# Performance work log

Measured on AMD Instinct MI355X. Metric: run time of the kernel, lower is better.

## Reference

```python
import jax, jax.numpy as jnp
import numpy as np

N_NODES = 100000
N_EDGES = 1600000
IN_DIM, HID_DIM, OUT_DIM = 128, 64, 32


def gcn_conv(x, edge_index, W, b, n_nodes):
    """PyG GCNConv: add self-loops, symmetric deg^-1/2 normalization,
    linear transform, gather->scatter-sum aggregation, then bias."""
    loops = jnp.arange(n_nodes, dtype=edge_index.dtype)
    src = jnp.concatenate([edge_index[0], loops])  # [E+N]
    dst = jnp.concatenate([edge_index[1], loops])  # [E+N]
    # degree over targets (includes self-loops)
    deg = jax.ops.segment_sum(jnp.ones_like(dst, dtype=x.dtype), dst,
                              num_segments=n_nodes)
    dinv = jnp.where(deg > 0, jax.lax.rsqrt(deg), 0.0)
    norm = dinv[src] * dinv[dst]                   # [E+N]
    h = x @ W                                      # [N, F_out]
    msg = h[src] * norm[:, None]                   # gather + scale
    out = jax.ops.segment_sum(msg, dst, num_segments=n_nodes)
    return out + b


def setup_inputs() -> dict:
    key = jax.random.key(0)
    k1, k2, k3, k4 = jax.random.split(key, 4)
    x = jax.random.normal(k1, (N_NODES, IN_DIM), dtype=jnp.float32)
    edge_index = jax.random.randint(k2, (2, N_EDGES), 0, N_NODES,
                                    dtype=jnp.int64)
    # Glorot-ish init for weights, zero bias (PyG default: glorot + zeros)
    W1 = jax.random.normal(k3, (IN_DIM, HID_DIM), dtype=jnp.float32) * (1.0 / np.sqrt(IN_DIM))
    b1 = jnp.zeros((HID_DIM,), dtype=jnp.float32)
    W2 = jax.random.normal(k4, (HID_DIM, OUT_DIM), dtype=jnp.float32) * (1.0 / np.sqrt(HID_DIM))
    b2 = jnp.zeros((OUT_DIM,), dtype=jnp.float32)
    return {"x": x, "edge_index": edge_index, "W1": W1, "b1": b1,
            "W2": W2, "b2": b2}


def reference(x, edge_index, W1, b1, W2, b2):
    n = x.shape[0]
    h = jax.nn.relu(gcn_conv(x, edge_index, W1, b1, n))
    return gcn_conv(h, edge_index, W2, b2, n)
```

## Files before the change

kernel.cpp:

```cpp
#include <hip/hip_runtime.h>


#define BLK 256
#define BLKC 1024
#define EPT 8
#define CITER 18
#define BSHIFT 10
#define NPB 1024
#define SLOTB 18432
#define NBMAX 128

typedef unsigned int uint_t;
typedef unsigned short ushort_t;
typedef __attribute__((ext_vector_type(2))) float v2f;
typedef __attribute__((ext_vector_type(8))) short bf16x8;
typedef __attribute__((ext_vector_type(4))) float f32x4;

__device__ __forceinline__ uint_t pkbf(float lo, float hi) {
    uint_t r;
    asm("v_cvt_pk_bf16_f32 %0, %1, %2" : "=v"(r) : "v"(lo), "v"(hi));
    return r;
}

__device__ __forceinline__ void pkadd(v2f& a0, v2f& a1, v2f& a2, v2f& a3, uint4 v) {
    v2f p;
    p.x = __uint_as_float(v.x << 16); p.y = __uint_as_float(v.x & 0xffff0000u); a0 += p;
    p.x = __uint_as_float(v.y << 16); p.y = __uint_as_float(v.y & 0xffff0000u); a1 += p;
    p.x = __uint_as_float(v.z << 16); p.y = __uint_as_float(v.z & 0xffff0000u); a2 += p;
    p.x = __uint_as_float(v.w << 16); p.y = __uint_as_float(v.w & 0xffff0000u); a3 += p;
}

__device__ __forceinline__ bool detect64(const int* __restrict__ idx) {
    int z = 0;
#pragma unroll
    for (int i = 1; i < 32; i += 2) z |= idx[i];
    return z == 0;
}

__global__ void k_part(const int* __restrict__ idx, int* __restrict__ bcursor,
                       int* __restrict__ edge_part,
                       const float* __restrict__ W1, const float* __restrict__ W2,
                       ushort_t* __restrict__ wt, int E, int nbuck, int PB) {
    if (blockIdx.x == PB) {
        int t = threadIdx.x;
        int n = t >> 2, q = t & 3;
        uint_t buf[16];
#pragma unroll
        for (int i = 0; i < 16; ++i) {
            float a = W1[(size_t)(32 * q + 2 * i) * 64 + n];
            float b = W1[(size_t)(32 * q + 2 * i + 1) * 64 + n];
            buf[i] = pkbf(a, b);
        }
#pragma unroll
        for (int i = 0; i < 4; ++i)
            ((uint4*)wt)[(size_t)n * 16 + q * 4 + i] = *(uint4*)&buf[4 * i];
        if (t < 128) {
            int n2 = t >> 2, q2 = t & 3;
            uint_t b2[8];
#pragma unroll
            for (int i = 0; i < 8; ++i) {
                float a = W2[(size_t)(16 * q2 + 2 * i) * 32 + n2];
                float b = W2[(size_t)(16 * q2 + 2 * i + 1) * 32 + n2];
                b2[i] = pkbf(a, b);
            }
#pragma unroll
            for (int i = 0; i < 2; ++i)
                ((uint4*)(wt + 8192))[(size_t)n2 * 8 + q2 * 2 + i] = *(uint4*)&b2[4 * i];
        }
        return;
    }
    __shared__ int h[NBMAX];
    __shared__ int rb[NBMAX];
    bool is64 = detect64(idx);
    int t = threadIdx.x, blk = blockIdx.x;
    for (int i = t; i < nbuck; i += BLK) h[i] = 0;
    __syncthreads();
    int base = blk * (BLK * EPT) + t;
    int dst[EPT], src[EPT], rk[EPT];
#pragma unroll
    for (int k = 0; k < EPT; ++k) {
        int e = base + k * BLK;
        if (e < E) {
            if (is64) {
                uint2 dv = ((const uint2*)idx)[(size_t)E + e];
                uint2 sv = ((const uint2*)idx)[e];
                dst[k] = (int)dv.x;
                src[k] = (int)sv.x;
            } else {
                dst[k] = idx[E + e];
                src[k] = idx[e];
            }
            rk[k] = atomicAdd(&h[dst[k] >> BSHIFT], 1);
        } else {
            dst[k] = -1;
        }
    }
    __syncthreads();
    for (int i = t; i < nbuck; i += BLK) {
        int c = h[i];
        rb[i] = c ? atomicAdd(&bcursor[i], c) : 0;
    }
    __syncthreads();
#pragma unroll
    for (int k = 0; k < EPT; ++k) {
        if (dst[k] >= 0) {
            int b = dst[k] >> BSHIFT;
            edge_part[(size_t)b * SLOTB + rb[b] + rk[k]] =
                src[k] | ((dst[k] & (NPB - 1)) << 17);
        }
    }
}

__global__ __launch_bounds__(BLKC) void k_csr(
        const int* __restrict__ edge_part, const int* __restrict__ bcursor,
        int* __restrict__ row_ptr, int* __restrict__ deg, float* __restrict__ dinv,
        int* __restrict__ csr_src, int N, int nbuck) {
    __shared__ int cnt[NPB];
    __shared__ int off[NPB];
    __shared__ int wsum[16];
    int b = blockIdx.x, t = threadIdx.x;
    int node0 = b << BSHIFT;
    int nn = min(NPB, N - node0);
    int m = bcursor[b];
    size_t ebase = (size_t)b * SLOTB;
    cnt[t] = 0;
    __syncthreads();
    int pp[CITER], rr[CITER];
#pragma unroll
    for (int it = 0; it < CITER; ++it) {
        int e = t + it * BLKC;
        if (e < m) {
            int p = edge_part[ebase + e];
            pp[it] = p;
            rr[it] = atomicAdd(&cnt[((unsigned)p) >> 17], 1);
        }
    }
    __syncthreads();
    int cown = cnt[t];
    int xi = cown;
#pragma unroll
    for (int d = 1; d < 64; d <<= 1) {
        int y = __shfl_up(xi, d, 64);
        if ((t & 63) >= d) xi += y;
    }
    if ((t & 63) == 63) wsum[t >> 6] = xi;
    __syncthreads();
    if (t < 16) {
        int wv = wsum[t];
#pragma unroll
        for (int d = 1; d < 16; d <<= 1) {
            int y = __shfl_up(wv, d, 64);
            if (t >= d) wv += y;
        }
        wsum[t] = wv;
    }
    __syncthreads();
    int excl = xi - cown + ((t >= 64) ? wsum[(t >> 6) - 1] : 0);
    off[t] = excl;
    if (t < nn) {
        row_ptr[node0 + t] = (int)(ebase + excl);
        deg[node0 + t] = cown;
        dinv[node0 + t] = rsqrtf((float)(cown + 1));
    }
    __syncthreads();
#pragma unroll
    for (int it = 0; it < CITER; ++it) {
        int e = t + it * BLKC;
        if (e < m) {
            int p = pp[it];
            int dlo = ((unsigned)p) >> 17;
            csr_src[ebase + off[dlo] + rr[it]] = p & 0x1FFFF;
        }
    }
}

__global__ __launch_bounds__(256) void k_gemm1(
        const float* __restrict__ x, const ushort_t* __restrict__ wt,
        const float* __restrict__ dinv, ushort_t* __restrict__ hs1, int N) {
    __shared__ ushort_t xb[64][136];
    __shared__ ushort_t wb[64][136];
    int t = threadIdx.x;
    int rbase = blockIdx.x * 64;
    for (int i = t; i < 1024; i += BLK) {
        int n = i >> 4, q = i & 15;
        uint4 v = ((const uint4*)wt)[i];
        *(uint4*)&wb[n][8 * q] = v;
    }
    for (int i = t; i < 2048; i += BLK) {
        int r = i >> 5, c4 = i & 31;
        int rr = rbase + r; if (rr >= N) rr = N - 1;
        float4 v = ((const float4*)x)[(size_t)rr * 32 + c4];
        uint2 p;
        p.x = pkbf(v.x, v.y);
        p.y = pkbf(v.z, v.w);
        *(uint2*)&xb[r][4 * c4] = p;
    }
    __syncthreads();
    int w = t >> 6, l = t & 63;
    int lane16 = l & 15, quad = l >> 4;
    int mrow = 16 * w + lane16;
    f32x4 acc0 = {0.f, 0.f, 0.f, 0.f}, acc1 = {0.f, 0.f, 0.f, 0.f};
    f32x4 acc2 = {0.f, 0.f, 0.f, 0.f}, acc3 = {0.f, 0.f, 0.f, 0.f};
#pragma unroll
    for (int kk = 0; kk < 4; ++kk) {
        int k0 = kk * 32 + quad * 8;
        bf16x8 a  = *(const bf16x8*)&xb[mrow][k0];
        bf16x8 b0 = *(const bf16x8*)&wb[lane16][k0];
        bf16x8 b1 = *(const bf16x8*)&wb[lane16 + 16][k0];
        bf16x8 b2 = *(const bf16x8*)&wb[lane16 + 32][k0];
        bf16x8 b3 = *(const bf16x8*)&wb[lane16 + 48][k0];
        acc0 = __builtin_amdgcn_mfma_f32_16x16x32_bf16(a, b0, acc0, 0, 0, 0);
        acc1 = __builtin_amdgcn_mfma_f32_16x16x32_bf16(a, b1, acc1, 0, 0, 0);
        acc2 = __builtin_amdgcn_mfma_f32_16x16x32_bf16(a, b2, acc2, 0, 0, 0);
        acc3 = __builtin_amdgcn_mfma_f32_16x16x32_bf16(a, b3, acc3, 0, 0, 0);
    }
    __syncthreads();
    int orow = 16 * w + quad * 4;
    float d0 = dinv[min(rbase + orow + 0, N - 1)];
    float d1 = dinv[min(rbase + orow + 1, N - 1)];
    float d2 = dinv[min(rbase + orow + 2, N - 1)];
    float d3 = dinv[min(rbase + orow + 3, N - 1)];
    uint_t u;
    u = pkbf(acc0.x * d0, acc0.y * d1);
    xb[orow + 0][lane16] = (ushort_t)u;  xb[orow + 1][lane16] = (ushort_t)(u >> 16);
    u = pkbf(acc0.z * d2, acc0.w * d3);
    xb[orow + 2][lane16] = (ushort_t)u;  xb[orow + 3][lane16] = (ushort_t)(u >> 16);
    u = pkbf(acc1.x * d0, acc1.y * d1);
    xb[orow + 0][lane16 + 16] = (ushort_t)u;  xb[orow + 1][lane16 + 16] = (ushort_t)(u >> 16);
    u = pkbf(acc1.z * d2, acc1.w * d3);
    xb[orow + 2][lane16 + 16] = (ushort_t)u;  xb[orow + 3][lane16 + 16] = (ushort_t)(u >> 16);
    u = pkbf(acc2.x * d0, acc2.y * d1);
    xb[orow + 0][lane16 + 32] = (ushort_t)u;  xb[orow + 1][lane16 + 32] = (ushort_t)(u >> 16);
    u = pkbf(acc2.z * d2, acc2.w * d3);
    xb[orow + 2][lane16 + 32] = (ushort_t)u;  xb[orow + 3][lane16 + 32] = (ushort_t)(u >> 16);
    u = pkbf(acc3.x * d0, acc3.y * d1);
    xb[orow + 0][lane16 + 48] = (ushort_t)u;  xb[orow + 1][lane16 + 48] = (ushort_t)(u >> 16);
    u = pkbf(acc3.z * d2, acc3.w * d3);
    xb[orow + 2][lane16 + 48] = (ushort_t)u;  xb[orow + 3][lane16 + 48] = (ushort_t)(u >> 16);
    __syncthreads();
    for (int i = t; i < 512; i += BLK) {
        int r = i >> 3, c8 = i & 7;
        int rr = rbase + r;
        if (rr < N) {
            uint4 v = *(const uint4*)&xb[r][8 * c8];
            *(uint4*)&hs1[(size_t)rr * 64 + 8 * c8] = v;
        }
    }
}

__global__ void k_agg1(const uint_t* __restrict__ hs1, const int* __restrict__ row_ptr,
                       const int* __restrict__ deg, const int* __restrict__ csr_src,
                       const float* __restrict__ dinv, const float* __restrict__ b1,
                       ushort_t* __restrict__ a1b, int N) {
    int lane = threadIdx.x & 63;
    int g = lane >> 3;
    int c = lane & 7;
    int wavebase = ((blockIdx.x * blockDim.x + threadIdx.x) >> 6) * 8;
    int node = wavebase + g;
    bool alive = node < N;
    int nodeC = alive ? node : N - 1;
    const uint4* H = (const uint4*)hs1;
    float dn = dinv[nodeC];
    int beg = row_ptr[nodeC];
    int tot = alive ? deg[nodeC] : 0;
    uint4 selfv = H[(size_t)nodeC * 8 + c];
    int gbase = lane & 0x38;
    int wtot = tot;
    wtot = max(wtot, __shfl_xor(wtot, 8, 64));
    wtot = max(wtot, __shfl_xor(wtot, 16, 64));
    wtot = max(wtot, __shfl_xor(wtot, 32, 64));
    int nch = (wtot + 7) >> 3;
    v2f a0 = {0.f, 0.f}, a1_ = {0.f, 0.f}, a2 = {0.f, 0.f}, a3 = {0.f, 0.f};
    uint4 vA[8], vB[8];
    auto ISSUE = [&](uint4 (&vv)[8], int i) {
        int base = 8 * i;
        int jal = (base + c < tot) ? csr_src[beg + base + c] : 0;
#pragma unroll
        for (int e = 0; e < 8; ++e) {
            int j = __shfl(jal, gbase + e, 64);
            if (base + e < tot) vv[e] = H[(size_t)j * 8 + c];
        }
    };
    auto CONSUME = [&](uint4 (&vv)[8], int i) {
        int base = 8 * i;
#pragma unroll
        for (int e = 0; e < 8; ++e)
            if (base + e < tot) pkadd(a0, a1_, a2, a3, vv[e]);
    };
    if (nch > 0) {
        ISSUE(vA, 0);
        int i = 1;
        for (; i + 1 < nch; i += 2) {
            ISSUE(vB, i);     CONSUME(vA, i - 1);
            ISSUE(vA, i + 1); CONSUME(vB, i);
        }
        if (i < nch) { ISSUE(vB, i); CONSUME(vA, i - 1); CONSUME(vB, i); }
        else          CONSUME(vA, i - 1);
    }
    pkadd(a0, a1_, a2, a3, selfv);
    if (alive) {
        const float4* B = (const float4*)b1;
        float4 bv0 = B[2 * c], bv1 = B[2 * c + 1];
        float o0 = fmaxf(fmaf(a0.x, dn, bv0.x), 0.f);
        float o1 = fmaxf(fmaf(a0.y, dn, bv0.y), 0.f);
        float o2 = fmaxf(fmaf(a1_.x, dn, bv0.z), 0.f);
        float o3 = fmaxf(fmaf(a1_.y, dn, bv0.w), 0.f);
        float o4 = fmaxf(fmaf(a2.x, dn, bv1.x), 0.f);
        float o5 = fmaxf(fmaf(a2.y, dn, bv1.y), 0.f);
        float o6 = fmaxf(fmaf(a3.x, dn, bv1.z), 0.f);
        float o7 = fmaxf(fmaf(a3.y, dn, bv1.w), 0.f);
        uint4 o;
        o.x = pkbf(o0, o1);
        o.y = pkbf(o2, o3);
        o.z = pkbf(o4, o5);
        o.w = pkbf(o6, o7);
        ((uint4*)a1b)[(size_t)node * 8 + c] = o;
    }
}

__global__ __launch_bounds__(256) void k_gemm2(
        const ushort_t* __restrict__ a1b, const ushort_t* __restrict__ wt,
        const float* __restrict__ dinv, ushort_t* __restrict__ hs2, int N) {
    __shared__ ushort_t ab[64][72];
    __shared__ ushort_t wb[32][72];
    int t = threadIdx.x;
    int rbase = blockIdx.x * 64;
    for (int i = t; i < 256; i += BLK) {
        int n = i >> 3, q = i & 7;
        uint4 v = ((const uint4*)(wt + 8192))[i];
        *(uint4*)&wb[n][8 * q] = v;
    }
    for (int i = t; i < 512; i += BLK) {
        int r = i >> 3, c8 = i & 7;
        int rr = rbase + r; if (rr >= N) rr = N - 1;
        uint4 v = ((const uint4*)a1b)[(size_t)rr * 8 + c8];
        *(uint4*)&ab[r][8 * c8] = v;
    }
    __syncthreads();
    int w = t >> 6, l = t & 63;
    int lane16 = l & 15, quad = l >> 4;
    int mrow = 16 * w + lane16;
    f32x4 acc0 = {0.f, 0.f, 0.f, 0.f}, acc1 = {0.f, 0.f, 0.f, 0.f};
#pragma unroll
    for (int kk = 0; kk < 2; ++kk) {
        int k0 = kk * 32 + quad * 8;
        bf16x8 a  = *(const bf16x8*)&ab[mrow][k0];
        bf16x8 b0 = *(const bf16x8*)&wb[lane16][k0];
        bf16x8 b1 = *(const bf16x8*)&wb[lane16 + 16][k0];
        acc0 = __builtin_amdgcn_mfma_f32_16x16x32_bf16(a, b0, acc0, 0, 0, 0);
        acc1 = __builtin_amdgcn_mfma_f32_16x16x32_bf16(a, b1, acc1, 0, 0, 0);
    }
    __syncthreads();
    int orow = 16 * w + quad * 4;
    float d0 = dinv[min(rbase + orow + 0, N - 1)];
    float d1 = dinv[min(rbase + orow + 1, N - 1)];
    float d2 = dinv[min(rbase + orow + 2, N - 1)];
    float d3 = dinv[min(rbase + orow + 3, N - 1)];
    uint_t u;
    u = pkbf(acc0.x * d0, acc0.y * d1);
    ab[orow + 0][lane16] = (ushort_t)u;  ab[orow + 1][lane16] = (ushort_t)(u >> 16);
    u = pkbf(acc0.z * d2, acc0.w * d3);
    ab[orow + 2][lane16] = (ushort_t)u;  ab[orow + 3][lane16] = (ushort_t)(u >> 16);
    u = pkbf(acc1.x * d0, acc1.y * d1);
    ab[orow + 0][lane16 + 16] = (ushort_t)u;  ab[orow + 1][lane16 + 16] = (ushort_t)(u >> 16);
    u = pkbf(acc1.z * d2, acc1.w * d3);
    ab[orow + 2][lane16 + 16] = (ushort_t)u;  ab[orow + 3][lane16 + 16] = (ushort_t)(u >> 16);
    __syncthreads();
    for (int i = t; i < 256; i += BLK) {
        int r = i >> 2, c4 = i & 3;
        int rr = rbase + r;
        if (rr < N) {
            uint4 v = *(const uint4*)&ab[r][8 * c4];
            *(uint4*)&hs2[(size_t)rr * 32 + 8 * c4] = v;
        }
    }
}

__global__ void k_agg2(const uint_t* __restrict__ hs2, const int* __restrict__ row_ptr,
                       const int* __restrict__ deg, const int* __restrict__ csr_src,
                       const float* __restrict__ dinv, const float* __restrict__ b2,
                       float* __restrict__ out, int N) {
    int lane = threadIdx.x & 63;
    int g = lane >> 2;
    int c = lane & 3;
    int wavebase = ((blockIdx.x * blockDim.x + threadIdx.x) >> 6) * 16;
    int node = wavebase + g;
    bool alive = node < N;
    int nodeC = alive ? node : N - 1;
    const uint4* H = (const uint4*)hs2;
    float dn = dinv[nodeC];
    int beg = row_ptr[nodeC];
    int tot = alive ? deg[nodeC] : 0;
    uint4 selfv = H[(size_t)nodeC * 4 + c];
    int gbase = lane & 0x3C;
    int wtot = tot;
    wtot = max(wtot, __shfl_xor(wtot, 4, 64));
    wtot = max(wtot, __shfl_xor(wtot, 8, 64));
    wtot = max(wtot, __shfl_xor(wtot, 16, 64));
    wtot = max(wtot, __shfl_xor(wtot, 32, 64));
    int nch = (wtot + 3) >> 2;
    v2f a0 = {0.f, 0.f}, a1_ = {0.f, 0.f}, a2 = {0.f, 0.f}, a3 = {0.f, 0.f};
    uint4 vA[4], vB[4];
    auto ISSUE = [&](uint4 (&vv)[4], int i) {
        int base = 4 * i;
        int jal = (base + c < tot) ? csr_src[beg + base + c] : 0;
#pragma unroll
        for (int e = 0; e < 4; ++e) {
            int j = __shfl(jal, gbase + e, 64);
            if (base + e < tot) vv[e] = H[(size_t)j * 4 + c];
        }
    };
    auto CONSUME = [&](uint4 (&vv)[4], int i) {
        int base = 4 * i;
#pragma unroll
        for (int e = 0; e < 4; ++e)
            if (base + e < tot) pkadd(a0, a1_, a2, a3, vv[e]);
    };
    if (nch > 0) {
        ISSUE(vA, 0);
        int i = 1;
        for (; i + 1 < nch; i += 2) {
            ISSUE(vB, i);     CONSUME(vA, i - 1);
            ISSUE(vA, i + 1); CONSUME(vB, i);
        }
        if (i < nch) { ISSUE(vB, i); CONSUME(vA, i - 1); CONSUME(vB, i); }
        else          CONSUME(vA, i - 1);
    }
    pkadd(a0, a1_, a2, a3, selfv);
    if (alive) {
        const float4* B = (const float4*)b2;
        float4 bv0 = B[2 * c], bv1 = B[2 * c + 1];
        float4 o0, o1;
        o0.x = fmaf(a0.x, dn, bv0.x);
        o0.y = fmaf(a0.y, dn, bv0.y);
        o0.z = fmaf(a1_.x, dn, bv0.z);
        o0.w = fmaf(a1_.y, dn, bv0.w);
        o1.x = fmaf(a2.x, dn, bv1.x);
        o1.y = fmaf(a2.y, dn, bv1.y);
        o1.z = fmaf(a3.x, dn, bv1.z);
        o1.w = fmaf(a3.y, dn, bv1.w);
        float4* O = (float4*)out;
        O[(size_t)node * 8 + 2 * c] = o0;
        O[(size_t)node * 8 + 2 * c + 1] = o1;
    }
}

extern "C" void kernel_launch(void* const* d_in, const int* in_sizes, int n_in,
                              void* d_out, int out_size, void* d_ws, size_t ws_size,
                              hipStream_t stream) {
    const float* x  = (const float*)d_in[0];
    const int*   idx = (const int*)d_in[1];
    const float* W1 = (const float*)d_in[2];
    const float* b1 = (const float*)d_in[3];
    const float* W2 = (const float*)d_in[4];
    const float* b2 = (const float*)d_in[5];
    float* out = (float*)d_out;

    const int N = in_sizes[0] / 128;
    const int E = in_sizes[1] / 2;
    const int nbuck = (N + NPB - 1) >> BSHIFT;
    const int PB = (E + BLK * EPT - 1) / (BLK * EPT);

    char* ws = (char*)d_ws;
    size_t off = 0;
    auto alloc = [&](size_t bytes) -> char* {
        char* p = ws + off;
        off = (off + bytes + 255) & ~(size_t)255;
        return p;
    };
    float* dinv     = (float*)alloc((size_t)N * 4);
    int*   row_ptr  = (int*)alloc((size_t)N * 4);
    int*   deg      = (int*)alloc((size_t)N * 4);
    int*   bcursor  = (int*)alloc((size_t)nbuck * 4);
    ushort_t* wt    = (ushort_t*)alloc((size_t)(8192 + 2048) * 2);
    int*   csr_src  = (int*)alloc((size_t)nbuck * SLOTB * 4);
    size_t ep_bytes = (size_t)nbuck * SLOTB * 4;
    size_t h1_bytes = (size_t)N * 64 * 2;
    int*   edge_part = (int*)alloc(ep_bytes > h1_bytes ? ep_bytes : h1_bytes);
    ushort_t* a1b   = (ushort_t*)alloc((size_t)N * 64 * 2);
    ushort_t* hs1   = (ushort_t*)edge_part;
    ushort_t* hs2   = hs1;

    hipMemsetAsync(bcursor, 0, (size_t)nbuck * 4, stream);
    k_part<<<PB + 1, BLK, 0, stream>>>(idx, bcursor, edge_part, W1, W2, wt,
                                       E, nbuck, PB);
    k_csr<<<nbuck, BLKC, 0, stream>>>(edge_part, bcursor, row_ptr, deg, dinv,
                                      csr_src, N, nbuck);
    k_gemm1<<<(N + 63) / 64, BLK, 0, stream>>>(x, wt, dinv, hs1, N);
    k_agg1<<<(N * 8 + BLK - 1) / BLK, BLK, 0, stream>>>(
        (const uint_t*)hs1, row_ptr, deg, csr_src, dinv, b1, a1b, N);
    k_gemm2<<<(N + 63) / 64, BLK, 0, stream>>>(a1b, wt, dinv, hs2, N);
    k_agg2<<<(N * 4 + BLK - 1) / BLK, BLK, 0, stream>>>(
        (const uint_t*)hs2, row_ptr, deg, csr_src, dinv, b2, out, N);
}
```

Before: 214.3 us.

## Shrink CSR buckets and use a zero sentinel row for branchless aggregation

Halves the node bucket size (512 nodes per bucket, smaller slot capacity). This gives more k_csr blocks, fewer per-thread iterations and a smaller edge scratch area, with only half the 1024 threads active in the scan phase. The aggregation kernels drop the double-buffered issue/consume pipeline and the per-edge bounds checks. Padding lanes now gather a zero row appended at index N of the hs buffers, which the GEMM kernels write. This removes divergent predication but loses the explicit software prefetch overlap between chunks.

```diff
diff --git a/kernel.cpp b/kernel.cpp
--- a/kernel.cpp
+++ b/kernel.cpp
@@ -4,11 +4,11 @@
 #define BLK 256
 #define BLKC 1024
 #define EPT 8
-#define CITER 18
-#define BSHIFT 10
-#define NPB 1024
-#define SLOTB 18432
-#define NBMAX 128
+#define CITER 10
+#define BSHIFT 9
+#define NPB 512
+#define SLOTB 10240
+#define NBMAX 256
 
 typedef unsigned int uint_t;
 typedef unsigned short ushort_t;
@@ -117,13 +117,13 @@
         int* __restrict__ csr_src, int N, int nbuck) {
     __shared__ int cnt[NPB];
     __shared__ int off[NPB];
-    __shared__ int wsum[16];
+    __shared__ int wsum[8];
     int b = blockIdx.x, t = threadIdx.x;
     int node0 = b << BSHIFT;
     int nn = min(NPB, N - node0);
     int m = bcursor[b];
     size_t ebase = (size_t)b * SLOTB;
-    cnt[t] = 0;
+    if (t < NPB) cnt[t] = 0;
     __syncthreads();
     int pp[CITER], rr[CITER];
 #pragma unroll
@@ -136,31 +136,36 @@
         }
     }
     __syncthreads();
-    int cown = cnt[t];
-    int xi = cown;
-#pragma unroll
-    for (int d = 1; d < 64; d <<= 1) {
-        int y = __shfl_up(xi, d, 64);
-        if ((t & 63) >= d) xi += y;
-    }
-    if ((t & 63) == 63) wsum[t >> 6] = xi;
-    __syncthreads();
-    if (t < 16) {
+    int cown = 0, xi = 0;
+    if (t < NPB) {
+        cown = cnt[t];
+        xi = cown;
+#pragma unroll
+        for (int d = 1; d < 64; d <<= 1) {
+            int y = __shfl_up(xi, d, 64);
+            if ((t & 63) >= d) xi += y;
+        }
+        if ((t & 63) == 63) wsum[t >> 6] = xi;
+    }
+    __syncthreads();
+    if (t < 8) {
         int wv = wsum[t];
 #pragma unroll
-        for (int d = 1; d < 16; d <<= 1) {
+        for (int d = 1; d < 8; d <<= 1) {
             int y = __shfl_up(wv, d, 64);
             if (t >= d) wv += y;
         }
         wsum[t] = wv;
     }
     __syncthreads();
-    int excl = xi - cown + ((t >= 64) ? wsum[(t >> 6) - 1] : 0);
-    off[t] = excl;
-    if (t < nn) {
-        row_ptr[node0 + t] = (int)(ebase + excl);
-        deg[node0 + t] = cown;
-        dinv[node0 + t] = rsqrtf((float)(cown + 1));
+    if (t < NPB) {
+        int excl = xi - cown + ((t >= 64) ? wsum[(t >> 6) - 1] : 0);
+        off[t] = excl;
+        if (t < nn) {
+            row_ptr[node0 + t] = (int)(ebase + excl);
+            deg[node0 + t] = cown;
+            dinv[node0 + t] = rsqrtf((float)(cown + 1));
+        }
     }
     __syncthreads();
 #pragma unroll
@@ -181,6 +186,10 @@
     __shared__ ushort_t wb[64][136];
     int t = threadIdx.x;
     int rbase = blockIdx.x * 64;
+    if (blockIdx.x == 0 && t < 8) {
+        uint4 z = {0u, 0u, 0u, 0u};
+        ((uint4*)hs1)[(size_t)N * 8 + t] = z;
+    }
     for (int i = t; i < 1024; i += BLK) {
         int n = i >> 4, q = i & 15;
         uint4 v = ((const uint4*)wt)[i];
@@ -271,31 +280,18 @@
     wtot = max(wtot, __shfl_xor(wtot, 32, 64));
     int nch = (wtot + 7) >> 3;
     v2f a0 = {0.f, 0.f}, a1_ = {0.f, 0.f}, a2 = {0.f, 0.f}, a3 = {0.f, 0.f};
-    uint4 vA[8], vB[8];
-    auto ISSUE = [&](uint4 (&vv)[8], int i) {
+    for (int i = 0; i < nch; ++i) {
         int base = 8 * i;
-        int jal = (base + c < tot) ? csr_src[beg + base + c] : 0;
+        int jal = (base + c < tot) ? csr_src[beg + base + c] : N;
+        uint4 vv[8];
 #pragma unroll
         for (int e = 0; e < 8; ++e) {
             int j = __shfl(jal, gbase + e, 64);
-            if (base + e < tot) vv[e] = H[(size_t)j * 8 + c];
-        }
-    };
-    auto CONSUME = [&](uint4 (&vv)[8], int i) {
-        int base = 8 * i;
+            vv[e] = H[(size_t)j * 8 + c];
+        }
 #pragma unroll
         for (int e = 0; e < 8; ++e)
-            if (base + e < tot) pkadd(a0, a1_, a2, a3, vv[e]);
-    };
-    if (nch > 0) {
-        ISSUE(vA, 0);
-        int i = 1;
-        for (; i + 1 < nch; i += 2) {
-            ISSUE(vB, i);     CONSUME(vA, i - 1);
-            ISSUE(vA, i + 1); CONSUME(vB, i);
-        }
-        if (i < nch) { ISSUE(vB, i); CONSUME(vA, i - 1); CONSUME(vB, i); }
-        else          CONSUME(vA, i - 1);
+            pkadd(a0, a1_, a2, a3, vv[e]);
     }
     pkadd(a0, a1_, a2, a3, selfv);
     if (alive) {
@@ -325,6 +321,10 @@
     __shared__ ushort_t wb[32][72];
     int t = threadIdx.x;
     int rbase = blockIdx.x * 64;
+    if (blockIdx.x == 0 && t < 4) {
+        uint4 z = {0u, 0u, 0u, 0u};
+        ((uint4*)hs2)[(size_t)N * 4 + t] = z;
+    }
     for (int i = t; i < 256; i += BLK) {
         int n = i >> 3, q = i & 7;
         uint4 v = ((const uint4*)(wt + 8192))[i];
@@ -400,31 +400,18 @@
     wtot = max(wtot, __shfl_xor(wtot, 32, 64));
     int nch = (wtot + 3) >> 2;
     v2f a0 = {0.f, 0.f}, a1_ = {0.f, 0.f}, a2 = {0.f, 0.f}, a3 = {0.f, 0.f};
-    uint4 vA[4], vB[4];
-    auto ISSUE = [&](uint4 (&vv)[4], int i) {
+    for (int i = 0; i < nch; ++i) {
         int base = 4 * i;
-        int jal = (base + c < tot) ? csr_src[beg + base + c] : 0;
+        int jal = (base + c < tot) ? csr_src[beg + base + c] : N;
+        uint4 vv[4];
 #pragma unroll
         for (int e = 0; e < 4; ++e) {
             int j = __shfl(jal, gbase + e, 64);
-            if (base + e < tot) vv[e] = H[(size_t)j * 4 + c];
-        }
-    };
-    auto CONSUME = [&](uint4 (&vv)[4], int i) {
-        int base = 4 * i;
+            vv[e] = H[(size_t)j * 4 + c];
+        }
 #pragma unroll
         for (int e = 0; e < 4; ++e)
-            if (base + e < tot) pkadd(a0, a1_, a2, a3, vv[e]);
-    };
-    if (nch > 0) {
-        ISSUE(vA, 0);
-        int i = 1;
-        for (; i + 1 < nch; i += 2) {
-            ISSUE(vB, i);     CONSUME(vA, i - 1);
-            ISSUE(vA, i + 1); CONSUME(vB, i);
-        }
-        if (i < nch) { ISSUE(vB, i); CONSUME(vA, i - 1); CONSUME(vB, i); }
-        else          CONSUME(vA, i - 1);
+            pkadd(a0, a1_, a2, a3, vv[e]);
     }
     pkadd(a0, a1_, a2, a3, selfv);
     if (alive) {
@@ -475,7 +462,7 @@
     ushort_t* wt    = (ushort_t*)alloc((size_t)(8192 + 2048) * 2);
     int*   csr_src  = (int*)alloc((size_t)nbuck * SLOTB * 4);
     size_t ep_bytes = (size_t)nbuck * SLOTB * 4;
-    size_t h1_bytes = (size_t)N * 64 * 2;
+    size_t h1_bytes = (size_t)(N + 1) * 64 * 2;
     int*   edge_part = (int*)alloc(ep_bytes > h1_bytes ? ep_bytes : h1_bytes);
     ushort_t* a1b   = (ushort_t*)alloc((size_t)N * 64 * 2);
     ushort_t* hs1   = (ushort_t*)edge_part;
```

Result: faster. 207.5 us (-3.2%).
